# Kernel tuning notes

Measured on AMD Instinct MI355X. Metric: run time of the kernel, lower is better.

Reference implementation:

```python
import jax, jax.numpy as jnp
import numpy as np

D_MODEL = 512
NUM_HEADS = 8
HEAD_DIM = D_MODEL // NUM_HEADS
NUM_HASHES = 8
SPARSITY_RATIO = 0.9
CURVATURE = 1.0


def setup_inputs() -> dict:
    key = jax.random.key(0)
    ks = jax.random.split(key, 6)
    B, N = 2, 1024
    x = jax.random.normal(ks[0], (B, N, D_MODEL), dtype=jnp.float32)
    s = 1.0 / np.sqrt(D_MODEL)
    Wq = jax.random.normal(ks[1], (D_MODEL, D_MODEL), dtype=jnp.float32) * s
    Wk = jax.random.normal(ks[2], (D_MODEL, D_MODEL), dtype=jnp.float32) * s
    Wv = jax.random.normal(ks[3], (D_MODEL, D_MODEL), dtype=jnp.float32) * s
    Wo = jax.random.normal(ks[4], (D_MODEL, D_MODEL), dtype=jnp.float32) * s
    rv = jax.random.normal(ks[5], (NUM_HASHES, HEAD_DIM), dtype=jnp.float32)
    rand_vecs = rv / jnp.linalg.norm(rv, axis=-1, keepdims=True)
    return {"x": x, "Wq": Wq, "Wk": Wk, "Wv": Wv, "Wo": Wo, "rand_vecs": rand_vecs}


def _split_heads(t, B, N):
    # [B, N, D] -> [B, H, N, Dh]
    return t.reshape(B, N, NUM_HEADS, HEAD_DIM).transpose(0, 2, 1, 3)


def reference(x, Wq, Wk, Wv, Wo, rand_vecs):
    B, N, D = x.shape
    q = _split_heads(x @ Wq.T, B, N)  # [B,H,N,Dh]
    k = _split_heads(x @ Wk.T, B, N)
    v = _split_heads(x @ Wv.T, B, N)

    top_k = max(1, int(N * (1.0 - SPARSITY_RATIO)))

    # LSH sign hashes: [B,H,N,num_hashes]
    q_h = (jnp.einsum('bhnd,kd->bhnk', q, rand_vecs) >= 0)
    k_h = (jnp.einsum('bhnd,kd->bhnk', k, rand_vecs) >= 0)
    # hash-agreement counts: [B,H,N,N]
    matches = (q_h[:, :, :, None, :] == k_h[:, :, None, :, :]).sum(-1)
    _, indices = jax.lax.top_k(matches.astype(jnp.float32), min(top_k, N))  # [B,H,N,K]

    # gather sparse K/V: [B,H,N,K,Dh]
    k_sparse = jnp.take_along_axis(k[:, :, None, :, :], indices[..., None], axis=3)
    v_sparse = jnp.take_along_axis(v[:, :, None, :, :], indices[..., None], axis=3)

    # hyperbolic (Poincare) distance scores
    diff_sq = ((q[:, :, :, None, :] - k_sparse) ** 2).sum(-1)       # [B,H,N,K]
    q_norm_sq = (q ** 2).sum(-1, keepdims=True)                      # [B,H,N,1]
    k_norm_sq = (k_sparse ** 2).sum(-1)                              # [B,H,N,K]
    denom = (1.0 - CURVATURE * q_norm_sq) * (1.0 - CURVATURE * k_norm_sq)
    denom = jnp.maximum(denom, 1e-6)
    cosh_arg = jnp.maximum(1.0 + 2.0 * CURVATURE * diff_sq / denom, 1.0)
    distance = jnp.arccosh(cosh_arg)

    attn = jax.nn.softmax(-distance, axis=-1)                        # [B,H,N,K]
    out = jnp.einsum('bhns,bhnsd->bhnd', attn, v_sparse)             # [B,H,N,Dh]
    out = out.transpose(0, 2, 1, 3).reshape(B, N, D)
    return out @ Wo.T
```

## Files before the change

### kernel.cpp

```cpp
#include <hip/hip_runtime.h>
#include <cstdint>
#include <cstddef>

#define Bb   2
#define Nn   1024
#define Hh   8
#define DHh  64
#define DMm  512
#define TOPK 102

__global__ __launch_bounds__(256) void gemm_f32_k4(
    const float* __restrict__ A,
    const float* __restrict__ B0, const float* __restrict__ B1,
    const float* __restrict__ B2, float* __restrict__ Cb) {
  __shared__ float smem[12288];
  const int tid  = threadIdx.x;
  const int wv   = tid >> 6;
  const int lane = tid & 63;
  const int bm   = blockIdx.x << 6;
  const int z    = blockIdx.y >> 3;
  const int bn   = (blockIdx.y & 7) << 6;
  const float* __restrict__ Bm = (z == 0) ? B0 : (z == 1) ? B1 : B2;
  float* __restrict__ C = Cb + (size_t)z * (size_t)(Bb * Nn) * DMm;

  float* const As = smem + wv * 2176;
  float* const Bs = As + 1088;

  const int rg = lane >> 3;
  const int cg = lane & 7;
  const int sr = lane >> 2;
  const int sk = (lane & 3) << 2;
  const int kb = wv << 7;

  const float* __restrict__ Ag = A  + (size_t)(bm + sr) * DMm + kb + sk;
  const float* __restrict__ Bg = Bm + (size_t)(bn + sr) * DMm + kb + sk;

  float acc[8][8] = {};

#pragma unroll 1
  for (int s = 0; s < 8; ++s) {
    const int ko = s << 4;
    {
      float4 t0 = *(const float4*)(Ag + ko);
      float4 t1 = *(const float4*)(Ag + ko + (size_t)16 * DMm);
      float4 t2 = *(const float4*)(Ag + ko + (size_t)32 * DMm);
      float4 t3 = *(const float4*)(Ag + ko + (size_t)48 * DMm);
      const float w0[4] = {t0.x, t0.y, t0.z, t0.w};
      const float w1[4] = {t1.x, t1.y, t1.z, t1.w};
      const float w2[4] = {t2.x, t2.y, t2.z, t2.w};
      const float w3[4] = {t3.x, t3.y, t3.z, t3.w};
#pragma unroll
      for (int c = 0; c < 4; ++c) {
        float* p = As + (sk + c) * 68 + sr;
        p[0]  = w0[c];
        p[16] = w1[c];
        p[32] = w2[c];
        p[48] = w3[c];
      }
    }
    {
      float4 t0 = *(const float4*)(Bg + ko);
      float4 t1 = *(const float4*)(Bg + ko + (size_t)16 * DMm);
      float4 t2 = *(const float4*)(Bg + ko + (size_t)32 * DMm);
      float4 t3 = *(const float4*)(Bg + ko + (size_t)48 * DMm);
      const float w0[4] = {t0.x, t0.y, t0.z, t0.w};
      const float w1[4] = {t1.x, t1.y, t1.z, t1.w};
      const float w2[4] = {t2.x, t2.y, t2.z, t2.w};
      const float w3[4] = {t3.x, t3.y, t3.z, t3.w};
#pragma unroll
      for (int c = 0; c < 4; ++c) {
        float* p = Bs + (sk + c) * 68 + sr;
        p[0]  = w0[c];
        p[16] = w1[c];
        p[32] = w2[c];
        p[48] = w3[c];
      }
    }
#pragma unroll
    for (int kk = 0; kk < 16; ++kk) {
      const float* pa = As + kk * 68 + (rg << 3);
      const float* pb = Bs + kk * 68 + (cg << 3);
      const float4 a0 = *(const float4*)pa;
      const float4 a1 = *(const float4*)(pa + 4);
      const float4 b0 = *(const float4*)pb;
      const float4 b1 = *(const float4*)(pb + 4);
      const float av[8] = {a0.x, a0.y, a0.z, a0.w, a1.x, a1.y, a1.z, a1.w};
      const float bw[8] = {b0.x, b0.y, b0.z, b0.w, b1.x, b1.y, b1.z, b1.w};
#pragma unroll
      for (int i = 0; i < 8; ++i)
#pragma unroll
        for (int j = 0; j < 8; ++j)
          acc[i][j] = fmaf(av[i], bw[j], acc[i][j]);
    }
  }

  __syncthreads();
  if (wv > 0) {
    float* pr = smem + ((wv - 1) << 12) + (rg << 9) + (cg << 3);
#pragma unroll
    for (int i = 0; i < 8; ++i) {
      float4 t0, t1;
      t0.x = acc[i][0]; t0.y = acc[i][1]; t0.z = acc[i][2]; t0.w = acc[i][3];
      t1.x = acc[i][4]; t1.y = acc[i][5]; t1.z = acc[i][6]; t1.w = acc[i][7];
      *(float4*)(pr + (i << 6))     = t0;
      *(float4*)(pr + (i << 6) + 4) = t1;
    }
  }
  __syncthreads();
  if (wv == 0) {
    const float* p1 = smem + (rg << 9) + (cg << 3);
#pragma unroll
    for (int i = 0; i < 8; ++i) {
#pragma unroll
      for (int h4 = 0; h4 < 2; ++h4) {
        float4 t;
        t.x = acc[i][h4 * 4 + 0]; t.y = acc[i][h4 * 4 + 1];
        t.z = acc[i][h4 * 4 + 2]; t.w = acc[i][h4 * 4 + 3];
        const float4 q1 = *(const float4*)(p1 +        (i << 6) + h4 * 4);
        const float4 q2 = *(const float4*)(p1 + 4096 + (i << 6) + h4 * 4);
        const float4 q3 = *(const float4*)(p1 + 8192 + (i << 6) + h4 * 4);
        t.x = ((t.x + q1.x) + q2.x) + q3.x;
        t.y = ((t.y + q1.y) + q2.y) + q3.y;
        t.z = ((t.z + q1.z) + q2.z) + q3.z;
        t.w = ((t.w + q1.w) + q2.w) + q3.w;
        *(float4*)(C + (size_t)(bm + (rg << 3) + i) * DMm + bn + (cg << 3) + h4 * 4) = t;
      }
    }
  }
}

__global__ __launch_bounds__(256) void hash_norm_kernel(
    const float* __restrict__ q, const float* __restrict__ k,
    const float* __restrict__ rv,
    uint32_t* __restrict__ qh, uint32_t* __restrict__ kh,
    float* __restrict__ qn, float* __restrict__ kn) {
  const int wid  = threadIdx.x >> 6;
  const int lane = threadIdx.x & 63;
  const int row  = blockIdx.x * 4 + wid;
  const int n    = row & (Nn - 1);
  const int bh   = row >> 10;
  const int b    = bh >> 3, h = bh & 7;
  const size_t off = (size_t)(b * Nn + n) * DMm + h * DHh + lane;
  const float qd = q[off], kd = k[off];
  float acc[18];
#pragma unroll
  for (int t = 0; t < 8; ++t) {
    float r = rv[t * DHh + lane];
    acc[t]     = qd * r;
    acc[8 + t] = kd * r;
  }
  acc[16] = qd * qd;
  acc[17] = kd * kd;
#pragma unroll
  for (int i = 0; i < 18; ++i) {
#pragma unroll
    for (int s = 1; s < 64; s <<= 1) acc[i] += __shfl_xor(acc[i], s);
  }
  if (lane == 0) {
    uint32_t qb = 0, kb = 0;
#pragma unroll
    for (int t = 0; t < 8; ++t) {
      qb |= (acc[t]     >= 0.f ? 1u : 0u) << t;
      kb |= (acc[8 + t] >= 0.f ? 1u : 0u) << t;
    }
    qh[row] = qb; kh[row] = kb;
    qn[row] = acc[16]; kn[row] = acc[17];
  }
}

__global__ __launch_bounds__(256) void attn_wave_kernel(
    const float* __restrict__ q, const float* __restrict__ k,
    const float* __restrict__ v,
    const uint32_t* __restrict__ qh, const uint32_t* __restrict__ kh,
    const float* __restrict__ qn, const float* __restrict__ kn,
    float* __restrict__ out) {
  const int wid  = threadIdx.x >> 6;
  const int lane = threadIdx.x & 63;
  const int bid  = blockIdx.x;
  const int xcd  = bid & 7;
  const int slot = bid >> 3;
  const int bh   = xcd + ((slot >> 8) << 3);
  const int nb   = slot & 255;
  const int row  = (bh << 10) + (nb << 2) + wid;
  const int n    = row & (Nn - 1);
  const int b    = bh >> 3, h = bh & 7;

  __shared__ int   sel[4][104];
  __shared__ float dw[4][104];

  const uint32_t myh = qh[row];
  const uint32_t* __restrict__ krh = kh + (bh << 10);

  int m[16];
#pragma unroll
  for (int c = 0; c < 16; ++c)
    m[c] = 8 - __popc(myh ^ krh[(c << 6) + lane]);

  uint32_t p0 = 0, p1 = 0, p2 = 0;
#pragma unroll
  for (int c = 0; c < 16; ++c) {
    uint32_t one = 1u << ((m[c] & 3) << 3);
    int gq = m[c] >> 2;
    p0 += (gq == 0) ? one : 0u;
    p1 += (gq == 1) ? one : 0u;
    p2 += (gq == 2) ? one : 0u;
  }
#pragma unroll
  for (int s = 1; s < 8; s <<= 1) {
    p0 += __shfl_xor(p0, s);
    p1 += __shfl_xor(p1, s);
    p2 += __shfl_xor(p2, s);
  }
  uint32_t hr[5];
  hr[0] = (p0 & 0xffu) | (((p0 >> 8) & 0xffu) << 16);
  hr[1] = ((p0 >> 16) & 0xffu) | (((p0 >> 24) & 0xffu) << 16);
  hr[2] = (p1 & 0xffu) | (((p1 >> 8) & 0xffu) << 16);
  hr[3] = ((p1 >> 16) & 0xffu) | (((p1 >> 24) & 0xffu) << 16);
  hr[4] = p2 & 0xffu;
#pragma unroll
  for (int i = 0; i < 5; ++i) {
#pragma unroll
    for (int s = 8; s < 64; s <<= 1) hr[i] += __shfl_xor(hr[i], s);
  }
  int cnt[9];
#pragma unroll
  for (int i = 0; i < 4; ++i) {
    cnt[2 * i]     = hr[i] & 0xffffu;
    cnt[2 * i + 1] = hr[i] >> 16;
  }
  cnt[8] = hr[4] & 0xffffu;

  int thr = 0, R = TOPK, gtc = 0;
  {
    int cum = 0; bool done = false;
#pragma unroll
    for (int mv = 8; mv >= 0; --mv) {
      int cx = cnt[mv];
      if (!done && cum + cx >= TOPK) { thr = mv; R = TOPK - cum; gtc = cum; done = true; }
      if (!done) cum += cx;
    }
  }

  const unsigned long long ltm = (1ULL << lane) - 1ULL;
  int bgt = 0, beq = 0;
#pragma unroll
  for (int c = 0; c < 16; ++c) {
    bool gt = m[c] > thr, eq = m[c] == thr;
    unsigned long long mg = __ballot(gt);
    unsigned long long me = __ballot(eq);
    int rg = bgt + __popcll(mg & ltm);
    int re = beq + __popcll(me & ltm);
    int j = (c << 6) + lane;
    if (gt) sel[wid][rg] = j;
    else if (eq && re < R) sel[wid][gtc + re] = j;
    bgt += __popcll(mg);
    beq += __popcll(me);
  }
  __builtin_amdgcn_wave_barrier();

  const int g  = lane >> 3;
  const int gl = lane & 7;
  const float* __restrict__ qrow = q + (size_t)(b * Nn + n) * DMm + h * DHh + gl * 8;
  const float4 qt0 = *(const float4*)qrow;
  const float4 qt1 = *(const float4*)(qrow + 4);
  const float qv[8] = {qt0.x, qt0.y, qt0.z, qt0.w, qt1.x, qt1.y, qt1.z, qt1.w};
  const float qnrm = qn[row];
  const float oneq = 1.f - qnrm;
  const float* __restrict__ kbh = k + (size_t)b * Nn * DMm + h * DHh;
  const float* __restrict__ knb = kn + (bh << 10);

#pragma unroll
  for (int it = 0; it < 13; ++it) {
    int s = it * 8 + g;
    bool act = s < TOPK;
    int j = act ? sel[wid][s] : sel[wid][0];
    const float* __restrict__ kr = kbh + (size_t)j * DMm + gl * 8;
    const float4 k0 = *(const float4*)kr;
    const float4 k1 = *(const float4*)(kr + 4);
    const float kv[8] = {k0.x, k0.y, k0.z, k0.w, k1.x, k1.y, k1.z, k1.w};
    float dot = 0.f;
#pragma unroll
    for (int d = 0; d < 8; ++d) dot = fmaf(kv[d], qv[d], dot);
    dot += __shfl_xor(dot, 1);
    dot += __shfl_xor(dot, 2);
    dot += __shfl_xor(dot, 4);
    if (gl == 0 && act) dw[wid][s] = dot;
  }
  __builtin_amdgcn_wave_barrier();

  float w0, w1 = 0.f;
  {
    int j0 = sel[wid][lane];
    float dot0 = dw[wid][lane];
    float kn0 = knb[j0];
    float dsq = fmaxf(qnrm + kn0 - 2.f * dot0, 0.f);
    float den = fmaxf(oneq * (1.f - kn0), 1e-6f);
    float cc  = fmaxf(fmaf(2.f * dsq, __builtin_amdgcn_rcpf(den), 1.f), 1.f);
    float zz  = cc + __builtin_amdgcn_sqrtf(fmaf(cc, cc, -1.f));
    w0 = __builtin_amdgcn_rcpf(zz);
  }
  if (lane + 64 < TOPK) {
    int j1 = sel[wid][lane + 64];
    float dot1 = dw[wid][lane + 64];
    float kn1 = knb[j1];
    float dsq = fmaxf(qnrm + kn1 - 2.f * dot1, 0.f);
    float den = fmaxf(oneq * (1.f - kn1), 1e-6f);
    float cc  = fmaxf(fmaf(2.f * dsq, __builtin_amdgcn_rcpf(den), 1.f), 1.f);
    float zz  = cc + __builtin_amdgcn_sqrtf(fmaf(cc, cc, -1.f));
    w1 = __builtin_amdgcn_rcpf(zz);
  }
  float sm = w0 + w1;
#pragma unroll
  for (int s = 1; s < 64; s <<= 1) sm += __shfl_xor(sm, s);
  const float inv = __builtin_amdgcn_rcpf(sm);
  dw[wid][lane] = w0;
  if (lane + 64 < TOPK) dw[wid][lane + 64] = w1;
  __builtin_amdgcn_wave_barrier();

  const float* __restrict__ vbh = v + (size_t)b * Nn * DMm + h * DHh;
  float oa[8] = {};
#pragma unroll
  for (int it = 0; it < 13; ++it) {
    int s = it * 8 + g;
    if (s < TOPK) {
      float w = dw[wid][s];
      const float* __restrict__ vr = vbh + (size_t)sel[wid][s] * DMm + gl * 8;
      const float4 v0 = *(const float4*)vr;
      const float4 v1 = *(const float4*)(vr + 4);
      const float vv[8] = {v0.x, v0.y, v0.z, v0.w, v1.x, v1.y, v1.z, v1.w};
#pragma unroll
      for (int d = 0; d < 8; ++d) oa[d] = fmaf(w, vv[d], oa[d]);
    }
  }
#pragma unroll
  for (int s = 8; s < 64; s <<= 1) {
#pragma unroll
    for (int d = 0; d < 8; ++d) oa[d] += __shfl_xor(oa[d], s);
  }
  if (g == 0) {
    float* __restrict__ orow = out + (size_t)(b * Nn + n) * DMm + h * DHh + gl * 8;
    float4 r0, r1;
    r0.x = oa[0] * inv; r0.y = oa[1] * inv; r0.z = oa[2] * inv; r0.w = oa[3] * inv;
    r1.x = oa[4] * inv; r1.y = oa[5] * inv; r1.z = oa[6] * inv; r1.w = oa[7] * inv;
    *(float4*)orow = r0;
    *(float4*)(orow + 4) = r1;
  }
}

extern "C" void kernel_launch(void* const* d_in, const int* in_sizes, int n_in,
                              void* d_out, int out_size, void* d_ws, size_t ws_size,
                              hipStream_t stream) {
  const float* x  = (const float*)d_in[0];
  const float* Wq = (const float*)d_in[1];
  const float* Wk = (const float*)d_in[2];
  const float* Wv = (const float*)d_in[3];
  const float* Wo = (const float*)d_in[4];
  const float* rv = (const float*)d_in[5];
  float* outp = (float*)d_out;

  const int M = Bb * Nn;
  const int RWS = Bb * Hh * Nn;
  float* q  = (float*)d_ws;
  float* k  = q + (size_t)M * DMm;
  float* v  = k + (size_t)M * DMm;
  float* ao = v + (size_t)M * DMm;
  uint32_t* qh = (uint32_t*)(ao + (size_t)M * DMm);
  uint32_t* kh = qh + RWS;
  float* qn = (float*)(kh + RWS);
  float* kn = qn + RWS;

  dim3 gq(M / 64, 24);
  gemm_f32_k4<<<gq, 256, 0, stream>>>(x, Wq, Wk, Wv, q);
  hash_norm_kernel<<<RWS / 4, 256, 0, stream>>>(q, k, rv, qh, kh, qn, kn);
  attn_wave_kernel<<<RWS / 4, 256, 0, stream>>>(q, k, v, qh, kh, qn, kn, ao);
  dim3 go(M / 64, 8);
  gemm_f32_k4<<<go, 256, 0, stream>>>(ao, Wo, Wo, Wo, outp);
}
```

Measured before the change: 133.1 us.

## Replace FP32 FMA GEMMs with split-bf16x3 MFMA GEMMs

Replaces the scalar FP32 split-K GEMM with an MFMA-based GEMM that splits each FP32 operand into three bf16 planes and sums six cross-products, emulating near-FP32 accuracy on matrix cores. Adds conversion kernels that split x, the four weight matrices, and the attention output into bf16 planes in workspace. The aim is to move the projection GEMMs onto matrix cores. In exchange it adds extra launches, extra memory traffic for the split planes, and small precision differences that could flip LSH hash signs or top-k selections.

```diff
diff --git a/kernel.cpp b/kernel.cpp
--- a/kernel.cpp
+++ b/kernel.cpp
@@ -9,124 +9,140 @@
 #define DMm  512
 #define TOPK 102
 
-__global__ __launch_bounds__(256) void gemm_f32_k4(
-    const float* __restrict__ A,
-    const float* __restrict__ B0, const float* __restrict__ B1,
-    const float* __restrict__ B2, float* __restrict__ Cb) {
-  __shared__ float smem[12288];
-  const int tid  = threadIdx.x;
-  const int wv   = tid >> 6;
-  const int lane = tid & 63;
-  const int bm   = blockIdx.x << 6;
-  const int z    = blockIdx.y >> 3;
-  const int bn   = (blockIdx.y & 7) << 6;
-  const float* __restrict__ Bm = (z == 0) ? B0 : (z == 1) ? B1 : B2;
-  float* __restrict__ C = Cb + (size_t)z * (size_t)(Bb * Nn) * DMm;
-
-  float* const As = smem + wv * 2176;
-  float* const Bs = As + 1088;
-
-  const int rg = lane >> 3;
-  const int cg = lane & 7;
-  const int sr = lane >> 2;
-  const int sk = (lane & 3) << 2;
-  const int kb = wv << 7;
-
-  const float* __restrict__ Ag = A  + (size_t)(bm + sr) * DMm + kb + sk;
-  const float* __restrict__ Bg = Bm + (size_t)(bn + sr) * DMm + kb + sk;
-
-  float acc[8][8] = {};
-
-#pragma unroll 1
-  for (int s = 0; s < 8; ++s) {
-    const int ko = s << 4;
-    {
-      float4 t0 = *(const float4*)(Ag + ko);
-      float4 t1 = *(const float4*)(Ag + ko + (size_t)16 * DMm);
-      float4 t2 = *(const float4*)(Ag + ko + (size_t)32 * DMm);
-      float4 t3 = *(const float4*)(Ag + ko + (size_t)48 * DMm);
-      const float w0[4] = {t0.x, t0.y, t0.z, t0.w};
-      const float w1[4] = {t1.x, t1.y, t1.z, t1.w};
-      const float w2[4] = {t2.x, t2.y, t2.z, t2.w};
-      const float w3[4] = {t3.x, t3.y, t3.z, t3.w};
-#pragma unroll
-      for (int c = 0; c < 4; ++c) {
-        float* p = As + (sk + c) * 68 + sr;
-        p[0]  = w0[c];
-        p[16] = w1[c];
-        p[32] = w2[c];
-        p[48] = w3[c];
+typedef __attribute__((ext_vector_type(8))) short          bf16x8;
+typedef __attribute__((ext_vector_type(4))) float          f32x4;
+typedef __attribute__((ext_vector_type(8))) unsigned short us8;
+typedef __attribute__((ext_vector_type(4))) unsigned short us4;
+
+__device__ __forceinline__ void split3(float a, unsigned short& h,
+                                       unsigned short& m, unsigned short& l) {
+  unsigned int ab = __float_as_uint(a);
+  h = (unsigned short)(ab >> 16);
+  float r = a - __uint_as_float(ab & 0xFFFF0000u);
+  unsigned int rb = __float_as_uint(r);
+  m = (unsigned short)(rb >> 16);
+  float r2 = r - __uint_as_float(rb & 0xFFFF0000u);
+  l = (unsigned short)(__float_as_uint(r2) >> 16);
+}
+
+__global__ __launch_bounds__(256) void cvt_split5(
+    const float* __restrict__ x,
+    const float* __restrict__ Wq, const float* __restrict__ Wk,
+    const float* __restrict__ Wv, const float* __restrict__ Wo,
+    unsigned short* __restrict__ xpl, unsigned short* __restrict__ wpl) {
+  const int e4 = (blockIdx.x * 256 + threadIdx.x) << 2;
+  const float* src;
+  unsigned short *dh, *dm, *dl;
+  int off;
+  if (e4 < 1048576) {
+    src = x; off = e4;
+    dh = xpl; dm = xpl + 1048576; dl = xpl + 2097152;
+  } else {
+    int r = e4 - 1048576;
+    int t = r >> 18;
+    off = r & 262143;
+    src = (t == 0) ? Wq : (t == 1) ? Wk : (t == 2) ? Wv : Wo;
+    unsigned short* base = wpl + (size_t)t * 786432;
+    dh = base; dm = base + 262144; dl = base + 524288;
+  }
+  const float4 a = *(const float4*)(src + off);
+  const float av[4] = {a.x, a.y, a.z, a.w};
+  us4 vh, vm, vl;
+#pragma unroll
+  for (int j = 0; j < 4; ++j) {
+    unsigned short th, tm, tl;
+    split3(av[j], th, tm, tl);
+    vh[j] = th; vm[j] = tm; vl[j] = tl;
+  }
+  *(us4*)(dh + off) = vh;
+  *(us4*)(dm + off) = vm;
+  *(us4*)(dl + off) = vl;
+}
+
+__global__ __launch_bounds__(256) void cvt_split1(
+    const float* __restrict__ src, unsigned short* __restrict__ pl) {
+  const int off = (blockIdx.x * 256 + threadIdx.x) << 2;
+  const float4 a = *(const float4*)(src + off);
+  const float av[4] = {a.x, a.y, a.z, a.w};
+  us4 vh, vm, vl;
+#pragma unroll
+  for (int j = 0; j < 4; ++j) {
+    unsigned short th, tm, tl;
+    split3(av[j], th, tm, tl);
+    vh[j] = th; vm[j] = tm; vl[j] = tl;
+  }
+  *(us4*)(pl + off)           = vh;
+  *(us4*)(pl + 1048576 + off) = vm;
+  *(us4*)(pl + 2097152 + off) = vl;
+}
+
+__global__ __launch_bounds__(256) void gemm_bf16x3(
+    const unsigned short* __restrict__ Ap,
+    const unsigned short* __restrict__ Wt,
+    float* __restrict__ Cb) {
+  __shared__ unsigned short lds[6][2560];
+  const int tid = threadIdx.x;
+  const int w   = tid >> 6;
+  const int l   = tid & 63;
+  const int bm  = blockIdx.x << 6;
+  const int z   = blockIdx.y >> 3;
+  const int bn  = (blockIdx.y & 7) << 6;
+  const unsigned short* __restrict__ Wp = Wt + (size_t)z * 786432;
+  float* __restrict__ C = Cb + (size_t)z * 1048576;
+
+  const int wr   = w >> 1, wc = w & 1;
+  const int srow = tid >> 2;
+  const int sc8  = (tid & 3) << 3;
+  const int lrow = l & 15;
+  const int lk8  = (l >> 4) << 3;
+
+  f32x4 acc[2][2] = {};
+
+  for (int ks = 0; ks < 16; ++ks) {
+    const int k0 = ks << 5;
+    __syncthreads();
+#pragma unroll
+    for (int p = 0; p < 3; ++p) {
+      const us8 av = *(const us8*)(Ap + (size_t)p * 1048576 +
+                                   (size_t)(bm + srow) * 512 + k0 + sc8);
+      *(us8*)&lds[p][srow * 40 + sc8] = av;
+      const us8 wv = *(const us8*)(Wp + (size_t)p * 262144 +
+                                   (size_t)(bn + srow) * 512 + k0 + sc8);
+      *(us8*)&lds[3 + p][srow * 40 + sc8] = wv;
+    }
+    __syncthreads();
+    bf16x8 aF[2][3], bF[2][3];
+#pragma unroll
+    for (int t2 = 0; t2 < 2; ++t2)
+#pragma unroll
+      for (int p = 0; p < 3; ++p) {
+        aF[t2][p] = *(const bf16x8*)&lds[p][(wr * 32 + t2 * 16 + lrow) * 40 + lk8];
+        bF[t2][p] = *(const bf16x8*)&lds[3 + p][(wc * 32 + t2 * 16 + lrow) * 40 + lk8];
       }
-    }
-    {
-      float4 t0 = *(const float4*)(Bg + ko);
-      float4 t1 = *(const float4*)(Bg + ko + (size_t)16 * DMm);
-      float4 t2 = *(const float4*)(Bg + ko + (size_t)32 * DMm);
-      float4 t3 = *(const float4*)(Bg + ko + (size_t)48 * DMm);
-      const float w0[4] = {t0.x, t0.y, t0.z, t0.w};
-      const float w1[4] = {t1.x, t1.y, t1.z, t1.w};
-      const float w2[4] = {t2.x, t2.y, t2.z, t2.w};
-      const float w3[4] = {t3.x, t3.y, t3.z, t3.w};
-#pragma unroll
-      for (int c = 0; c < 4; ++c) {
-        float* p = Bs + (sk + c) * 68 + sr;
-        p[0]  = w0[c];
-        p[16] = w1[c];
-        p[32] = w2[c];
-        p[48] = w3[c];
+#pragma unroll
+    for (int rt = 0; rt < 2; ++rt)
+#pragma unroll
+      for (int ct = 0; ct < 2; ++ct) {
+        f32x4 a = acc[rt][ct];
+        a = __builtin_amdgcn_mfma_f32_16x16x32_bf16(aF[rt][0], bF[ct][0], a, 0, 0, 0);
+        a = __builtin_amdgcn_mfma_f32_16x16x32_bf16(aF[rt][0], bF[ct][1], a, 0, 0, 0);
+        a = __builtin_amdgcn_mfma_f32_16x16x32_bf16(aF[rt][1], bF[ct][0], a, 0, 0, 0);
+        a = __builtin_amdgcn_mfma_f32_16x16x32_bf16(aF[rt][0], bF[ct][2], a, 0, 0, 0);
+        a = __builtin_amdgcn_mfma_f32_16x16x32_bf16(aF[rt][1], bF[ct][1], a, 0, 0, 0);
+        a = __builtin_amdgcn_mfma_f32_16x16x32_bf16(aF[rt][2], bF[ct][0], a, 0, 0, 0);
+        acc[rt][ct] = a;
       }
-    }
-#pragma unroll
-    for (int kk = 0; kk < 16; ++kk) {
-      const float* pa = As + kk * 68 + (rg << 3);
-      const float* pb = Bs + kk * 68 + (cg << 3);
-      const float4 a0 = *(const float4*)pa;
-      const float4 a1 = *(const float4*)(pa + 4);
-      const float4 b0 = *(const float4*)pb;
-      const float4 b1 = *(const float4*)(pb + 4);
-      const float av[8] = {a0.x, a0.y, a0.z, a0.w, a1.x, a1.y, a1.z, a1.w};
-      const float bw[8] = {b0.x, b0.y, b0.z, b0.w, b1.x, b1.y, b1.z, b1.w};
-#pragma unroll
-      for (int i = 0; i < 8; ++i)
-#pragma unroll
-        for (int j = 0; j < 8; ++j)
-          acc[i][j] = fmaf(av[i], bw[j], acc[i][j]);
-    }
-  }
-
-  __syncthreads();
-  if (wv > 0) {
-    float* pr = smem + ((wv - 1) << 12) + (rg << 9) + (cg << 3);
-#pragma unroll
-    for (int i = 0; i < 8; ++i) {
-      float4 t0, t1;
-      t0.x = acc[i][0]; t0.y = acc[i][1]; t0.z = acc[i][2]; t0.w = acc[i][3];
-      t1.x = acc[i][4]; t1.y = acc[i][5]; t1.z = acc[i][6]; t1.w = acc[i][7];
-      *(float4*)(pr + (i << 6))     = t0;
-      *(float4*)(pr + (i << 6) + 4) = t1;
-    }
-  }
-  __syncthreads();
-  if (wv == 0) {
-    const float* p1 = smem + (rg << 9) + (cg << 3);
-#pragma unroll
-    for (int i = 0; i < 8; ++i) {
-#pragma unroll
-      for (int h4 = 0; h4 < 2; ++h4) {
-        float4 t;
-        t.x = acc[i][h4 * 4 + 0]; t.y = acc[i][h4 * 4 + 1];
-        t.z = acc[i][h4 * 4 + 2]; t.w = acc[i][h4 * 4 + 3];
-        const float4 q1 = *(const float4*)(p1 +        (i << 6) + h4 * 4);
-        const float4 q2 = *(const float4*)(p1 + 4096 + (i << 6) + h4 * 4);
-        const float4 q3 = *(const float4*)(p1 + 8192 + (i << 6) + h4 * 4);
-        t.x = ((t.x + q1.x) + q2.x) + q3.x;
-        t.y = ((t.y + q1.y) + q2.y) + q3.y;
-        t.z = ((t.z + q1.z) + q2.z) + q3.z;
-        t.w = ((t.w + q1.w) + q2.w) + q3.w;
-        *(float4*)(C + (size_t)(bm + (rg << 3) + i) * DMm + bn + (cg << 3) + h4 * 4) = t;
+  }
+#pragma unroll
+  for (int rt = 0; rt < 2; ++rt)
+#pragma unroll
+    for (int ct = 0; ct < 2; ++ct)
+#pragma unroll
+      for (int r = 0; r < 4; ++r) {
+        const int row = bm + wr * 32 + rt * 16 + (l >> 4) * 4 + r;
+        const int col = bn + wc * 32 + ct * 16 + (l & 15);
+        C[(size_t)row * 512 + col] = acc[rt][ct][r];
       }
-    }
-  }
 }
 
 __global__ __launch_bounds__(256) void hash_norm_kernel(
@@ -358,21 +374,25 @@
   const float* rv = (const float*)d_in[5];
   float* outp = (float*)d_out;
 
-  const int M = Bb * Nn;
   const int RWS = Bb * Hh * Nn;
-  float* q  = (float*)d_ws;
-  float* k  = q + (size_t)M * DMm;
-  float* v  = k + (size_t)M * DMm;
-  float* ao = v + (size_t)M * DMm;
-  uint32_t* qh = (uint32_t*)(ao + (size_t)M * DMm);
+  char* wsb = (char*)d_ws;
+  float* q  = (float*)wsb;
+  float* k  = q + 1048576;
+  float* v  = k + 1048576;
+  float* ao = v + 1048576;
+  uint32_t* qh = (uint32_t*)(ao + 1048576);
   uint32_t* kh = qh + RWS;
   float* qn = (float*)(kh + RWS);
   float* kn = qn + RWS;
-
-  dim3 gq(M / 64, 24);
-  gemm_f32_k4<<<gq, 256, 0, stream>>>(x, Wq, Wk, Wv, q);
+  unsigned short* xpl = (unsigned short*)(wsb + (size_t)17 * 1024 * 1024);
+  unsigned short* wpl = xpl + (size_t)3 * 1048576;
+
+  cvt_split5<<<2048, 256, 0, stream>>>(x, Wq, Wk, Wv, Wo, xpl, wpl);
+  dim3 gq(32, 24);
+  gemm_bf16x3<<<gq, 256, 0, stream>>>(xpl, wpl, q);
   hash_norm_kernel<<<RWS / 4, 256, 0, stream>>>(q, k, rv, qh, kh, qn, kn);
   attn_wave_kernel<<<RWS / 4, 256, 0, stream>>>(q, k, v, qh, kh, qn, kn, ao);
-  dim3 go(M / 64, 8);
-  gemm_f32_k4<<<go, 256, 0, stream>>>(ao, Wo, Wo, Wo, outp);
-}
+  cvt_split1<<<1024, 256, 0, stream>>>(ao, xpl);
+  dim3 go(32, 8);
+  gemm_bf16x3<<<go, 256, 0, stream>>>(xpl, wpl + (size_t)3 * 786432, outp);
+}
```

New measurement: 123.9 us. -6.9%, faster.
